# Kernel tuning notes

Hardware: AMD Instinct MI355X
Metric: run time of the kernel (lower is better)

Reference implementation:

```python
import jax, jax.numpy as jnp
import numpy as np

B, N, C, H = 1, 1024, 384, 12
DK, DV, P, PV = 16, 16, 4, 4  # scalar key/value dims, query/value points
POINT_KEY_DIM = 4

def setup_inputs() -> dict:
    key = jax.random.key(0)
    ks = jax.random.split(key, 12)
    s = 0.02
    x = jax.random.normal(ks[0], (B, N, C), dtype=jnp.float32)
    # random orthonormal frames via QR
    A = jax.random.normal(ks[1], (B, N, 3, 3), dtype=jnp.float32)
    rotations, _ = jnp.linalg.qr(A)
    translations = jax.random.normal(ks[2], (B, N, 3), dtype=jnp.float32) * 10.0
    Wq  = jax.random.normal(ks[3], (C, H * DK), dtype=jnp.float32) * s
    Wk  = jax.random.normal(ks[4], (C, H * DK), dtype=jnp.float32) * s
    Wv  = jax.random.normal(ks[5], (C, H * DV), dtype=jnp.float32) * s
    Wqp = jax.random.normal(ks[6], (C, H * P * 3), dtype=jnp.float32) * s
    Wkp = jax.random.normal(ks[7], (C, H * P * 3), dtype=jnp.float32) * s
    Wvp = jax.random.normal(ks[8], (C, H * PV * 3), dtype=jnp.float32) * s
    Wout = jax.random.normal(ks[9], (H * DV + H * PV, C), dtype=jnp.float32) * s
    bout = jnp.zeros((C,), dtype=jnp.float32)
    return {"x": x, "rotations": rotations, "translations": translations,
            "Wq": Wq, "Wk": Wk, "Wv": Wv, "Wqp": Wqp, "Wkp": Wkp, "Wvp": Wvp,
            "Wout": Wout, "bout": bout}

def reference(x, rotations, translations, Wq, Wk, Wv, Wqp, Wkp, Wvp, Wout, bout):
    b, n, c = x.shape
    h = H
    # scalar q/k/v: (b,n,h,d)
    qs = (x @ Wq).reshape(b, n, h, DK)
    ks_ = (x @ Wk).reshape(b, n, h, DK)
    vs = (x @ Wv).reshape(b, n, h, DV)
    # local points: (b,n,h,p,3)
    qp = (x @ Wqp).reshape(b, n, h, P, 3)
    kp = (x @ Wkp).reshape(b, n, h, P, 3)
    vp = (x @ Wvp).reshape(b, n, h, PV, 3)
    t = translations[:, :, None, None, :]
    # rotate to global frame
    qpg = jnp.einsum('bnij,bnhpj->bnhpi', rotations, qp) + t
    kpg = jnp.einsum('bnij,bnhpj->bnhpi', rotations, kp) + t
    vpg = jnp.einsum('bnij,bnhpj->bnhpi', rotations, vp) + t
    # scalar attention logits (b,h,i,j)
    attn_scalar = jnp.einsum('bihd,bjhd->bhij', qs, ks_)
    # squared distances summed over points and coords, expanded to avoid (n,n,h,p,3) diff tensor
    q2 = (qpg ** 2).sum((-1, -2))          # (b,n,h)
    k2 = (kpg ** 2).sum((-1, -2))          # (b,n,h)
    qk = jnp.einsum('bihpc,bjhpc->bhij', qpg, kpg)
    dist_sq = (q2.transpose(0, 2, 1)[:, :, :, None]
               + k2.transpose(0, 2, 1)[:, :, None, :]
               - 2.0 * qk)                 # (b,h,i,j)
    gamma = np.sqrt(2.0 / (9.0 * POINT_KEY_DIM)).astype(np.float32)
    inv_sqrt_dk = np.float32(1.0 / np.sqrt(DK))
    logits = (attn_scalar - 0.5 * gamma * dist_sq) * inv_sqrt_dk
    w = jax.nn.softmax(logits, axis=-1)    # (b,h,i,j)
    # scalar output: (b,n,h*dv)
    out_scalar = jnp.einsum('bhij,bjhd->bihd', w, vs).reshape(b, n, h * DV)
    # point output in global frame, then back to local frame of residue i
    out_pts_g = jnp.einsum('bhij,bjhpc->bihpc', w, vpg)   # (b,n,h,pv,3)
    centered = out_pts_g - t
    out_pts_local = jnp.einsum('bnji,bnhpj->bnhpi', rotations, centered)
    out_pts_norm = jnp.sqrt((out_pts_local ** 2).sum(-1)).reshape(b, n, h * PV)
    out = jnp.concatenate([out_scalar, out_pts_norm], axis=-1)
    return out @ Wout + bout
```

## Files before the change

kernel.cpp:

```cpp
#include <hip/hip_runtime.h>
#include <math.h>

#define N_TOK 1024
#define C_DIM 384
#define H_NUM 12
#define PCOLS 1024
#define Q0 0
#define K0 192
#define V0 384
#define QP0 576
#define KP0 720
#define VP0 864
#define ATT_W 240
#define COEF 0.11785113019775792f
#define ISD 0.25f
#define CC2 (COEF * ISD)
#define NZ 4
#define OKV_V16 896
#define OKV_VP 1408
#define OKV_K2 2176
#define TILE_U 2240
#define TILE_PAD 2304

typedef _Float16 f16x2 __attribute__((ext_vector_type(2)));
typedef __fp16   p16x2 __attribute__((ext_vector_type(2)));
union U32H2 { unsigned int u; f16x2 f; p16x2 p; };
__device__ __forceinline__ f16x2 as_h2(unsigned int v) { U32H2 x; x.u = v; return x.f; }
__device__ __forceinline__ unsigned int pkh(float a, float b) {
    U32H2 x; x.p = __builtin_amdgcn_cvt_pkrtz(a, b); return x.u;
}
__device__ __forceinline__ f16x2 pkf(float a, float b) {
    U32H2 x; x.p = __builtin_amdgcn_cvt_pkrtz(a, b); return x.f;
}

__global__ __launch_bounds__(512) void k_proj(
    const float* __restrict__ x,
    const float* __restrict__ Wq, const float* __restrict__ Wk, const float* __restrict__ Wv,
    const float* __restrict__ Wqp, const float* __restrict__ Wkp, const float* __restrict__ Wvp,
    float* __restrict__ P)
{
    __shared__ unsigned int xs[8][72];
    __shared__ unsigned int wsh[8][64];
    int tid = threadIdx.x;
    int i0 = blockIdx.x * 64, c0 = blockIdx.y * 64;
    int sdp = tid & 7, slr = tid >> 3;
    int wdp = tid >> 6, wcc = tid & 63;
    int ty = tid >> 4, tx = tid & 15;

    int col = c0 + wcc;
    const float* Wb; int od, cb;
    if (col < 192)       { Wb = Wq;  od = 192; cb = col; }
    else if (col < 384)  { Wb = Wk;  od = 192; cb = col - 192; }
    else if (col < 576)  { Wb = Wv;  od = 192; cb = col - 384; }
    else if (col < 720)  { Wb = Wqp; od = 144; cb = col - 576; }
    else if (col < 864)  { Wb = Wkp; od = 144; cb = col - 720; }
    else if (col < 1008) { Wb = Wvp; od = 144; cb = col - 864; }
    else                 { Wb = nullptr; od = 0; cb = 0; }

    const float* xr = x + (i0 + slr) * C_DIM;

    float2 xa = *(const float2*)(xr + sdp * 2);
    float w0 = Wb ? Wb[(2 * wdp) * od + cb] : 0.f;
    float w1 = Wb ? Wb[(2 * wdp + 1) * od + cb] : 0.f;
    float acc[2][4] = {};

    for (int it = 0; it < 24; ++it) {
        xs[sdp][slr] = pkh(xa.x, xa.y);
        wsh[wdp][wcc] = pkh(w0, w1);
        __syncthreads();
        if (it < 23) {
            xa = *(const float2*)(xr + (it + 1) * 16 + sdp * 2);
            w0 = Wb ? Wb[((it + 1) * 16 + 2 * wdp) * od + cb] : 0.f;
            w1 = Wb ? Wb[((it + 1) * 16 + 2 * wdp + 1) * od + cb] : 0.f;
        }
#pragma unroll
        for (int dp = 0; dp < 8; ++dp) {
            uint2 au = *(const uint2*)&xs[dp][ty * 2];
            uint4 bu = *(const uint4*)&wsh[dp][tx * 4];
            unsigned int aa[2] = {au.x, au.y};
            unsigned int bb[4] = {bu.x, bu.y, bu.z, bu.w};
#pragma unroll
            for (int r = 0; r < 2; ++r)
#pragma unroll
                for (int c = 0; c < 4; ++c)
                    acc[r][c] = __builtin_amdgcn_fdot2(as_h2(aa[r]), as_h2(bb[c]), acc[r][c], false);
        }
        __syncthreads();
    }
#pragma unroll
    for (int r = 0; r < 2; ++r)
        *(float4*)(P + (i0 + ty * 2 + r) * PCOLS + c0 + tx * 4) =
            make_float4(acc[r][0], acc[r][1], acc[r][2], acc[r][3]);
}

__global__ __launch_bounds__(256) void k_prep(
    const float* __restrict__ P, const float* __restrict__ rot, const float* __restrict__ trans,
    unsigned int* __restrict__ KVT, unsigned int* __restrict__ Qh, float* __restrict__ qcg)
{
    __shared__ float kb[29 * 128];
    __shared__ float qb[28 * 128];
    __shared__ float vb[28 * 128];
    __shared__ float qcb[128];
    int h = blockIdx.y, nb = blockIdx.x;
    int tid = threadIdx.x;
    int nl = tid & 127, role = tid >> 7;
    int n = nb * 128 + nl;
    const float* R = rot + n * 9;
    float R00 = R[0], R01 = R[1], R02 = R[2];
    float R10 = R[3], R11 = R[4], R12 = R[5];
    float R20 = R[6], R21 = R[7], R22 = R[8];
    float t0 = trans[n * 3 + 0], t1 = trans[n * 3 + 1], t2 = trans[n * 3 + 2];

    if (role == 0) {
        const float* kr = P + n * PCOLS + K0 + h * 16;
#pragma unroll
        for (int d = 0; d < 16; ++d) kb[d * 128 + nl] = kr[d];
        const float* kp = P + n * PCOLS + KP0 + h * 12;
        float k2 = 0.f;
#pragma unroll
        for (int pt = 0; pt < 4; ++pt) {
            float p0 = kp[pt * 3 + 0], p1 = kp[pt * 3 + 1], p2 = kp[pt * 3 + 2];
            float g0 = R00 * p0 + R01 * p1 + R02 * p2 + t0;
            float g1 = R10 * p0 + R11 * p1 + R12 * p2 + t1;
            float g2 = R20 * p0 + R21 * p1 + R22 * p2 + t2;
            kb[(16 + pt * 3 + 0) * 128 + nl] = g0;
            kb[(16 + pt * 3 + 1) * 128 + nl] = g1;
            kb[(16 + pt * 3 + 2) * 128 + nl] = g2;
            k2 += g0 * g0 + g1 * g1 + g2 * g2;
        }
        kb[28 * 128 + nl] = -CC2 * k2;
    } else {
        const float* qr = P + n * PCOLS + Q0 + h * 16;
#pragma unroll
        for (int d = 0; d < 16; ++d) qb[d * 128 + nl] = qr[d] * ISD;
        const float* qp = P + n * PCOLS + QP0 + h * 12;
        float q2 = 0.f;
#pragma unroll
        for (int pt = 0; pt < 4; ++pt) {
            float p0 = qp[pt * 3 + 0], p1 = qp[pt * 3 + 1], p2 = qp[pt * 3 + 2];
            float g0 = R00 * p0 + R01 * p1 + R02 * p2 + t0;
            float g1 = R10 * p0 + R11 * p1 + R12 * p2 + t1;
            float g2 = R20 * p0 + R21 * p1 + R22 * p2 + t2;
            qb[(16 + pt * 3 + 0) * 128 + nl] = g0 * (2.f * CC2);
            qb[(16 + pt * 3 + 1) * 128 + nl] = g1 * (2.f * CC2);
            qb[(16 + pt * 3 + 2) * 128 + nl] = g2 * (2.f * CC2);
            q2 += g0 * g0 + g1 * g1 + g2 * g2;
        }
        qcb[nl] = fmaf(-CC2, q2, -4.0f);
        const float* vr = P + n * PCOLS + V0 + h * 16;
#pragma unroll
        for (int d = 0; d < 16; ++d) vb[d * 128 + nl] = vr[d];
        const float* vp = P + n * PCOLS + VP0 + h * 12;
#pragma unroll
        for (int pt = 0; pt < 4; ++pt) {
            float p0 = vp[pt * 3 + 0], p1 = vp[pt * 3 + 1], p2 = vp[pt * 3 + 2];
            vb[(16 + pt * 3 + 0) * 128 + nl] = R00 * p0 + R01 * p1 + R02 * p2 + t0;
            vb[(16 + pt * 3 + 1) * 128 + nl] = R10 * p0 + R11 * p1 + R12 * p2 + t1;
            vb[(16 + pt * 3 + 2) * 128 + nl] = R20 * p0 + R21 * p1 + R22 * p2 + t2;
        }
    }
    __syncthreads();

    for (int u = tid; u < 2 * TILE_PAD; u += 256) {
        int tt = u / TILE_PAD, r = u % TILE_PAD;
        unsigned int val;
        if (r < OKV_V16) {
            int dp = r >> 6, j = r & 63;
            val = pkh(kb[(2 * dp) * 128 + tt * 64 + j], kb[(2 * dp + 1) * 128 + tt * 64 + j]);
        } else if (r < OKV_VP) {
            int idx = r - OKV_V16;
            int d = idx >> 5, jp = idx & 31;
            val = pkh(vb[d * 128 + tt * 64 + 2 * jp], vb[d * 128 + tt * 64 + 2 * jp + 1]);
        } else if (r < OKV_K2) {
            int idx = r - OKV_VP;
            int d = idx >> 6, j = idx & 63;
            val = __float_as_uint(vb[(16 + d) * 128 + tt * 64 + j]);
        } else if (r < TILE_U) {
            int j = r - OKV_K2;
            val = __float_as_uint(kb[28 * 128 + tt * 64 + j]);
        } else {
            val = 0u;
        }
        KVT[(h * 16 + nb * 2 + tt) * TILE_PAD + r] = val;
    }
    for (int u = tid; u < 14 * 128; u += 256) {
        int dp = u >> 7, n2 = u & 127;
        Qh[(h * 14 + dp) * 1024 + nb * 128 + n2] =
            pkh(qb[(2 * dp) * 128 + n2], qb[(2 * dp + 1) * 128 + n2]);
    }
    if (tid < 32) *(float4*)&qcg[h * 1024 + nb * 128 + tid * 4] = *(float4*)&qcb[tid * 4];
}

__global__ __launch_bounds__(256, 2) void k_attn(
    const unsigned int* __restrict__ KVT, const unsigned int* __restrict__ Qh,
    const float* __restrict__ qcg, float* __restrict__ part)
{
    __shared__ unsigned int KV[2][TILE_PAD];
    __shared__ float red[29 * 64];
    int tid = threadIdx.x;
    int lane = tid & 63, w = tid >> 6;
    int ty = tid >> 3, tx = tid & 7;

    int bid = blockIdx.x;
    int xcd = bid & 7, slot = bid >> 3;
    int pair = xcd * 6 + (slot >> 4);
    int bx = slot & 15;
    int h = pair % H_NUM;
    int z = pair / H_NUM;

    int i0 = bx * 64;
    const unsigned int* KVbase = KVT + (h * 16 + z * 4) * TILE_PAD;

    f16x2 q0p[14], q1p[14];
#pragma unroll
    for (int dp = 0; dp < 14; ++dp) {
        q0p[dp] = as_h2(Qh[(h * 14 + dp) * 1024 + i0 + ty * 2 + 0]);
        q1p[dp] = as_h2(Qh[(h * 14 + dp) * 1024 + i0 + ty * 2 + 1]);
    }
    float qc[2];
    {
        float2 qcv = *(const float2*)&qcg[h * 1024 + i0 + ty * 2];
        qc[0] = qcv.x; qc[1] = qcv.y;
    }

    int nst = (w == 0) ? 3 : 2;
    int gbase = (w == 0) ? 0 : 1 + w * 2;
#define STAGE(T) do { unsigned int* buf_ = KV[(T) & 1];                          \
        const unsigned int* sb_ = KVbase + (T) * TILE_PAD;                       \
        for (int m_ = 0; m_ < nst; ++m_) {                                       \
            int g_ = gbase + m_;                                                 \
            const unsigned int* src_ = sb_ + g_ * 256 + lane * 4;                \
            unsigned int* dst_ = buf_ + g_ * 256;                                \
            __builtin_amdgcn_global_load_lds(                                    \
                (const __attribute__((address_space(1))) void*)src_,             \
                (__attribute__((address_space(3))) void*)dst_, 16, 0, 0);        \
        } } while (0)

    STAGE(0);
    __syncthreads();

    float out[2][28] = {};
    float denom[2] = {};

    for (int t = 0; t < 4; ++t) {
        if (t < 3) STAGE(t + 1);
        const unsigned int* Kb = KV[t & 1];

        float s[2][8] = {};
#pragma unroll
        for (int dp = 0; dp < 14; ++dp) {
            uint4 a = *(const uint4*)&Kb[dp * 64 + tx * 8];
            uint4 b = *(const uint4*)&Kb[dp * 64 + tx * 8 + 4];
            unsigned int ka[8] = {a.x, a.y, a.z, a.w, b.x, b.y, b.z, b.w};
#pragma unroll
            for (int j = 0; j < 8; ++j) {
                s[0][j] = __builtin_amdgcn_fdot2(q0p[dp], as_h2(ka[j]), s[0][j], false);
                s[1][j] = __builtin_amdgcn_fdot2(q1p[dp], as_h2(ka[j]), s[1][j], false);
            }
        }
        const float* k2p = (const float*)&Kb[OKV_K2];
        float4 c0 = *(const float4*)&k2p[tx * 8];
        float4 c1 = *(const float4*)&k2p[tx * 8 + 4];
        float k2v[8] = {c0.x, c0.y, c0.z, c0.w, c1.x, c1.y, c1.z, c1.w};

        float p[2][8];
#pragma unroll
        for (int r = 0; r < 2; ++r) {
#pragma unroll
            for (int j = 0; j < 8; ++j) {
                p[r][j] = __expf(s[r][j] + k2v[j] + qc[r]);
                denom[r] += p[r][j];
            }
        }
        f16x2 pp[2][4];
#pragma unroll
        for (int r = 0; r < 2; ++r)
#pragma unroll
            for (int jp = 0; jp < 4; ++jp)
                pp[r][jp] = pkf(p[r][2 * jp], p[r][2 * jp + 1]);

#pragma unroll
        for (int d = 0; d < 16; ++d) {
            uint4 vv = *(const uint4*)&Kb[OKV_V16 + d * 32 + tx * 4];
#pragma unroll
            for (int r = 0; r < 2; ++r) {
                float acc = out[r][d];
                acc = __builtin_amdgcn_fdot2(pp[r][0], as_h2(vv.x), acc, false);
                acc = __builtin_amdgcn_fdot2(pp[r][1], as_h2(vv.y), acc, false);
                acc = __builtin_amdgcn_fdot2(pp[r][2], as_h2(vv.z), acc, false);
                acc = __builtin_amdgcn_fdot2(pp[r][3], as_h2(vv.w), acc, false);
                out[r][d] = acc;
            }
        }
#pragma unroll
        for (int d = 0; d < 12; ++d) {
            const float* vp = (const float*)&Kb[OKV_VP + d * 64];
            float4 v0 = *(const float4*)&vp[tx * 8];
            float4 v1 = *(const float4*)&vp[tx * 8 + 4];
            float va[8] = {v0.x, v0.y, v0.z, v0.w, v1.x, v1.y, v1.z, v1.w};
#pragma unroll
            for (int r = 0; r < 2; ++r) {
                float acc = out[r][16 + d];
#pragma unroll
                for (int j = 0; j < 8; ++j) acc = fmaf(p[r][j], va[j], acc);
                out[r][16 + d] = acc;
            }
        }
        __syncthreads();
    }

#pragma unroll
    for (int m = 1; m <= 4; m <<= 1) {
#pragma unroll
        for (int r = 0; r < 2; ++r) {
#pragma unroll
            for (int d = 0; d < 28; ++d) out[r][d] += __shfl_xor(out[r][d], m, 64);
            denom[r] += __shfl_xor(denom[r], m, 64);
        }
    }
    if (tx == 0) {
#pragma unroll
        for (int r = 0; r < 2; ++r) {
#pragma unroll
            for (int d = 0; d < 28; ++d) red[d * 64 + ty * 2 + r] = out[r][d];
            red[28 * 64 + ty * 2 + r] = denom[r];
        }
    }
    __syncthreads();
    for (int u = tid; u < 29 * 64; u += 256) {
        part[((z * H_NUM + h) * 29 + (u >> 6)) * N_TOK + i0 + (u & 63)] = red[u];
    }
}

__global__ __launch_bounds__(256) void k_comb(
    const float* __restrict__ part, const float* __restrict__ rot,
    const float* __restrict__ trans, float* __restrict__ att)
{
    int t = blockIdx.x * 256 + threadIdx.x;
    int h = t >> 10, i = t & 1023;
    float v[29];
#pragma unroll
    for (int c = 0; c < 29; ++c) {
        float s = 0.f;
#pragma unroll
        for (int z = 0; z < NZ; ++z)
            s += part[((z * H_NUM + h) * 29 + c) * N_TOK + i];
        v[c] = s;
    }
    float inv = 1.f / v[28];
    float* arow = att + i * ATT_W;
#pragma unroll
    for (int d = 0; d < 16; ++d) arow[h * 16 + d] = v[d] * inv;
    float t0 = trans[i * 3 + 0], t1 = trans[i * 3 + 1], t2v = trans[i * 3 + 2];
    const float* R = rot + i * 9;
#pragma unroll
    for (int p = 0; p < 4; ++p) {
        float c0 = v[16 + p * 3 + 0] * inv - t0;
        float c1 = v[16 + p * 3 + 1] * inv - t1;
        float c2 = v[16 + p * 3 + 2] * inv - t2v;
        float l0 = R[0] * c0 + R[3] * c1 + R[6] * c2;
        float l1 = R[1] * c0 + R[4] * c1 + R[7] * c2;
        float l2 = R[2] * c0 + R[5] * c1 + R[8] * c2;
        arow[192 + h * 4 + p] = sqrtf(l0 * l0 + l1 * l1 + l2 * l2);
    }
}

__global__ __launch_bounds__(256) void k_out(
    const float* __restrict__ att, const float* __restrict__ Wout,
    const float* __restrict__ bout, float* __restrict__ out)
{
    __shared__ float xs[64][17];
    __shared__ float wsh[16][64];
    int tid = threadIdx.x;
    int i0 = blockIdx.x * 64, c0 = blockIdx.y * 64;
    int lr = tid >> 2, lk = (tid & 3) * 4;
    int wr = tid >> 4, wc = (tid & 15) * 4;
    int ty = tid >> 4, tx = tid & 15;

    float4 xa = *(const float4*)(att + (i0 + lr) * ATT_W + lk);
    float4 wa = *(const float4*)(Wout + wr * C_DIM + c0 + wc);
    float acc[4][4] = {};

    for (int it = 0; it < 15; ++it) {
        xs[lr][lk + 0] = xa.x; xs[lr][lk + 1] = xa.y;
        xs[lr][lk + 2] = xa.z; xs[lr][lk + 3] = xa.w;
        *(float4*)&wsh[wr][wc] = wa;
        __syncthreads();
        if (it < 14) {
            xa = *(const float4*)(att + (i0 + lr) * ATT_W + (it + 1) * 16 + lk);
            wa = *(const float4*)(Wout + ((it + 1) * 16 + wr) * C_DIM + c0 + wc);
        }
#pragma unroll
        for (int kk = 0; kk < 16; ++kk) {
            float4 b = *(float4*)&wsh[kk][tx * 4];
            float a0 = xs[ty * 4 + 0][kk];
            float a1 = xs[ty * 4 + 1][kk];
            float a2 = xs[ty * 4 + 2][kk];
            float a3 = xs[ty * 4 + 3][kk];
            acc[0][0] = fmaf(a0, b.x, acc[0][0]); acc[0][1] = fmaf(a0, b.y, acc[0][1]);
            acc[0][2] = fmaf(a0, b.z, acc[0][2]); acc[0][3] = fmaf(a0, b.w, acc[0][3]);
            acc[1][0] = fmaf(a1, b.x, acc[1][0]); acc[1][1] = fmaf(a1, b.y, acc[1][1]);
            acc[1][2] = fmaf(a1, b.z, acc[1][2]); acc[1][3] = fmaf(a1, b.w, acc[1][3]);
            acc[2][0] = fmaf(a2, b.x, acc[2][0]); acc[2][1] = fmaf(a2, b.y, acc[2][1]);
            acc[2][2] = fmaf(a2, b.z, acc[2][2]); acc[2][3] = fmaf(a2, b.w, acc[2][3]);
            acc[3][0] = fmaf(a3, b.x, acc[3][0]); acc[3][1] = fmaf(a3, b.y, acc[3][1]);
            acc[3][2] = fmaf(a3, b.z, acc[3][2]); acc[3][3] = fmaf(a3, b.w, acc[3][3]);
        }
        __syncthreads();
    }
    float4 bb = *(const float4*)(bout + c0 + tx * 4);
#pragma unroll
    for (int r = 0; r < 4; ++r) {
        *(float4*)(out + (i0 + ty * 4 + r) * C_DIM + c0 + tx * 4) =
            make_float4(acc[r][0] + bb.x, acc[r][1] + bb.y, acc[r][2] + bb.z, acc[r][3] + bb.w);
    }
}

extern "C" void kernel_launch(void* const* d_in, const int* in_sizes, int n_in,
                              void* d_out, int out_size, void* d_ws, size_t ws_size,
                              hipStream_t stream) {
    const float* x     = (const float*)d_in[0];
    const float* rot   = (const float*)d_in[1];
    const float* trans = (const float*)d_in[2];
    const float* Wq    = (const float*)d_in[3];
    const float* Wk    = (const float*)d_in[4];
    const float* Wv    = (const float*)d_in[5];
    const float* Wqp   = (const float*)d_in[6];
    const float* Wkp   = (const float*)d_in[7];
    const float* Wvp   = (const float*)d_in[8];
    const float* Wout  = (const float*)d_in[9];
    const float* bout  = (const float*)d_in[10];
    float* out = (float*)d_out;

    float* ws = (float*)d_ws;
    float* P            = ws;
    unsigned int* KVT   = (unsigned int*)(P + N_TOK * PCOLS);
    unsigned int* Qh    = KVT + H_NUM * 16 * TILE_PAD;
    float* qcg          = (float*)(Qh + H_NUM * 14 * 1024);
    float* part         = qcg + H_NUM * 1024;
    float* att          = part + NZ * H_NUM * 29 * 1024;

    k_proj<<<dim3(16, 16), 512, 0, stream>>>(x, Wq, Wk, Wv, Wqp, Wkp, Wvp, P);
    k_prep<<<dim3(8, 12), 256, 0, stream>>>(P, rot, trans, KVT, Qh, qcg);
    k_attn<<<768, 256, 0, stream>>>(KVT, Qh, qcg, part);
    k_comb<<<48, 256, 0, stream>>>(part, rot, trans, att);
    k_out<<<dim3(16, 6), 256, 0, stream>>>(att, Wout, bout, out);
}
```

Before: 81.15 us.

## Fuse partial-combine into output projection and split prep across more blocks

```diff
diff --git a/kernel.cpp b/kernel.cpp
--- a/kernel.cpp
+++ b/kernel.cpp
@@ -97,14 +97,14 @@
     const float* __restrict__ P, const float* __restrict__ rot, const float* __restrict__ trans,
     unsigned int* __restrict__ KVT, unsigned int* __restrict__ Qh, float* __restrict__ qcg)
 {
-    __shared__ float kb[29 * 128];
-    __shared__ float qb[28 * 128];
-    __shared__ float vb[28 * 128];
-    __shared__ float qcb[128];
+    __shared__ float kb[29 * 64];
+    __shared__ float qb[28 * 64];
+    __shared__ float vb[28 * 64];
+    __shared__ float qcb[64];
     int h = blockIdx.y, nb = blockIdx.x;
     int tid = threadIdx.x;
-    int nl = tid & 127, role = tid >> 7;
-    int n = nb * 128 + nl;
+    int nl = tid & 63, role = tid >> 6;
+    int n = nb * 64 + nl;
     const float* R = rot + n * 9;
     float R00 = R[0], R01 = R[1], R02 = R[2];
     float R10 = R[3], R11 = R[4], R12 = R[5];
@@ -114,7 +114,7 @@
     if (role == 0) {
         const float* kr = P + n * PCOLS + K0 + h * 16;
 #pragma unroll
-        for (int d = 0; d < 16; ++d) kb[d * 128 + nl] = kr[d];
+        for (int d = 0; d < 16; ++d) kb[d * 64 + nl] = kr[d];
         const float* kp = P + n * PCOLS + KP0 + h * 12;
         float k2 = 0.f;
 #pragma unroll
@@ -123,16 +123,16 @@
             float g0 = R00 * p0 + R01 * p1 + R02 * p2 + t0;
             float g1 = R10 * p0 + R11 * p1 + R12 * p2 + t1;
             float g2 = R20 * p0 + R21 * p1 + R22 * p2 + t2;
-            kb[(16 + pt * 3 + 0) * 128 + nl] = g0;
-            kb[(16 + pt * 3 + 1) * 128 + nl] = g1;
-            kb[(16 + pt * 3 + 2) * 128 + nl] = g2;
+            kb[(16 + pt * 3 + 0) * 64 + nl] = g0;
+            kb[(16 + pt * 3 + 1) * 64 + nl] = g1;
+            kb[(16 + pt * 3 + 2) * 64 + nl] = g2;
             k2 += g0 * g0 + g1 * g1 + g2 * g2;
         }
-        kb[28 * 128 + nl] = -CC2 * k2;
-    } else {
+        kb[28 * 64 + nl] = -CC2 * k2;
+    } else if (role == 1) {
         const float* qr = P + n * PCOLS + Q0 + h * 16;
 #pragma unroll
-        for (int d = 0; d < 16; ++d) qb[d * 128 + nl] = qr[d] * ISD;
+        for (int d = 0; d < 16; ++d) qb[d * 64 + nl] = qr[d] * ISD;
         const float* qp = P + n * PCOLS + QP0 + h * 12;
         float q2 = 0.f;
 #pragma unroll
@@ -141,54 +141,56 @@
             float g0 = R00 * p0 + R01 * p1 + R02 * p2 + t0;
             float g1 = R10 * p0 + R11 * p1 + R12 * p2 + t1;
             float g2 = R20 * p0 + R21 * p1 + R22 * p2 + t2;
-            qb[(16 + pt * 3 + 0) * 128 + nl] = g0 * (2.f * CC2);
-            qb[(16 + pt * 3 + 1) * 128 + nl] = g1 * (2.f * CC2);
-            qb[(16 + pt * 3 + 2) * 128 + nl] = g2 * (2.f * CC2);
+            qb[(16 + pt * 3 + 0) * 64 + nl] = g0 * (2.f * CC2);
+            qb[(16 + pt * 3 + 1) * 64 + nl] = g1 * (2.f * CC2);
+            qb[(16 + pt * 3 + 2) * 64 + nl] = g2 * (2.f * CC2);
             q2 += g0 * g0 + g1 * g1 + g2 * g2;
         }
         qcb[nl] = fmaf(-CC2, q2, -4.0f);
+    } else if (role == 2) {
         const float* vr = P + n * PCOLS + V0 + h * 16;
 #pragma unroll
-        for (int d = 0; d < 16; ++d) vb[d * 128 + nl] = vr[d];
+        for (int d = 0; d < 16; ++d) vb[d * 64 + nl] = vr[d];
+    } else {
         const float* vp = P + n * PCOLS + VP0 + h * 12;
 #pragma unroll
         for (int pt = 0; pt < 4; ++pt) {
             float p0 = vp[pt * 3 + 0], p1 = vp[pt * 3 + 1], p2 = vp[pt * 3 + 2];
-            vb[(16 + pt * 3 + 0) * 128 + nl] = R00 * p0 + R01 * p1 + R02 * p2 + t0;
-            vb[(16 + pt * 3 + 1) * 128 + nl] = R10 * p0 + R11 * p1 + R12 * p2 + t1;
-            vb[(16 + pt * 3 + 2) * 128 + nl] = R20 * p0 + R21 * p1 + R22 * p2 + t2;
+            vb[(16 + pt * 3 + 0) * 64 + nl] = R00 * p0 + R01 * p1 + R02 * p2 + t0;
+            vb[(16 + pt * 3 + 1) * 64 + nl] = R10 * p0 + R11 * p1 + R12 * p2 + t1;
+            vb[(16 + pt * 3 + 2) * 64 + nl] = R20 * p0 + R21 * p1 + R22 * p2 + t2;
         }
     }
     __syncthreads();
 
-    for (int u = tid; u < 2 * TILE_PAD; u += 256) {
-        int tt = u / TILE_PAD, r = u % TILE_PAD;
+    unsigned int* dstT = KVT + (h * 16 + nb) * TILE_PAD;
+    for (int r = tid; r < TILE_PAD; r += 256) {
         unsigned int val;
         if (r < OKV_V16) {
             int dp = r >> 6, j = r & 63;
-            val = pkh(kb[(2 * dp) * 128 + tt * 64 + j], kb[(2 * dp + 1) * 128 + tt * 64 + j]);
+            val = pkh(kb[(2 * dp) * 64 + j], kb[(2 * dp + 1) * 64 + j]);
         } else if (r < OKV_VP) {
             int idx = r - OKV_V16;
             int d = idx >> 5, jp = idx & 31;
-            val = pkh(vb[d * 128 + tt * 64 + 2 * jp], vb[d * 128 + tt * 64 + 2 * jp + 1]);
+            val = pkh(vb[d * 64 + 2 * jp], vb[d * 64 + 2 * jp + 1]);
         } else if (r < OKV_K2) {
             int idx = r - OKV_VP;
             int d = idx >> 6, j = idx & 63;
-            val = __float_as_uint(vb[(16 + d) * 128 + tt * 64 + j]);
+            val = __float_as_uint(vb[(16 + d) * 64 + j]);
         } else if (r < TILE_U) {
             int j = r - OKV_K2;
-            val = __float_as_uint(kb[28 * 128 + tt * 64 + j]);
+            val = __float_as_uint(kb[28 * 64 + j]);
         } else {
             val = 0u;
         }
-        KVT[(h * 16 + nb * 2 + tt) * TILE_PAD + r] = val;
-    }
-    for (int u = tid; u < 14 * 128; u += 256) {
-        int dp = u >> 7, n2 = u & 127;
-        Qh[(h * 14 + dp) * 1024 + nb * 128 + n2] =
-            pkh(qb[(2 * dp) * 128 + n2], qb[(2 * dp + 1) * 128 + n2]);
-    }
-    if (tid < 32) *(float4*)&qcg[h * 1024 + nb * 128 + tid * 4] = *(float4*)&qcb[tid * 4];
+        dstT[r] = val;
+    }
+    for (int u = tid; u < 14 * 64; u += 256) {
+        int dp = u >> 6, n2 = u & 63;
+        Qh[(h * 14 + dp) * 1024 + nb * 64 + n2] =
+            pkh(qb[(2 * dp) * 64 + n2], qb[(2 * dp + 1) * 64 + n2]);
+    }
+    if (tid < 16) *(float4*)&qcg[h * 1024 + nb * 64 + tid * 4] = *(float4*)&qcb[tid * 4];
 }
 
 __global__ __launch_bounds__(256, 2) void k_attn(
@@ -332,71 +334,77 @@
     }
 }
 
-__global__ __launch_bounds__(256) void k_comb(
+__global__ __launch_bounds__(256) void k_outc(
     const float* __restrict__ part, const float* __restrict__ rot,
-    const float* __restrict__ trans, float* __restrict__ att)
-{
-    int t = blockIdx.x * 256 + threadIdx.x;
-    int h = t >> 10, i = t & 1023;
-    float v[29];
-#pragma unroll
-    for (int c = 0; c < 29; ++c) {
-        float s = 0.f;
-#pragma unroll
-        for (int z = 0; z < NZ; ++z)
-            s += part[((z * H_NUM + h) * 29 + c) * N_TOK + i];
-        v[c] = s;
-    }
-    float inv = 1.f / v[28];
-    float* arow = att + i * ATT_W;
-#pragma unroll
-    for (int d = 0; d < 16; ++d) arow[h * 16 + d] = v[d] * inv;
-    float t0 = trans[i * 3 + 0], t1 = trans[i * 3 + 1], t2v = trans[i * 3 + 2];
-    const float* R = rot + i * 9;
-#pragma unroll
-    for (int p = 0; p < 4; ++p) {
-        float c0 = v[16 + p * 3 + 0] * inv - t0;
-        float c1 = v[16 + p * 3 + 1] * inv - t1;
-        float c2 = v[16 + p * 3 + 2] * inv - t2v;
-        float l0 = R[0] * c0 + R[3] * c1 + R[6] * c2;
-        float l1 = R[1] * c0 + R[4] * c1 + R[7] * c2;
-        float l2 = R[2] * c0 + R[5] * c1 + R[8] * c2;
-        arow[192 + h * 4 + p] = sqrtf(l0 * l0 + l1 * l1 + l2 * l2);
-    }
-}
-
-__global__ __launch_bounds__(256) void k_out(
-    const float* __restrict__ att, const float* __restrict__ Wout,
+    const float* __restrict__ trans, const float* __restrict__ Wout,
     const float* __restrict__ bout, float* __restrict__ out)
 {
-    __shared__ float xs[64][17];
+    __shared__ float ab[64][241];
+    __shared__ float den[64][13];
     __shared__ float wsh[16][64];
     int tid = threadIdx.x;
     int i0 = blockIdx.x * 64, c0 = blockIdx.y * 64;
-    int lr = tid >> 2, lk = (tid & 3) * 4;
+
+    for (int u = tid; u < 64 * 12; u += 256) {
+        int r = u & 63, h = u >> 6;
+        float s = 0.f;
+#pragma unroll
+        for (int z = 0; z < NZ; ++z)
+            s += part[((z * H_NUM + h) * 29 + 28) * N_TOK + i0 + r];
+        den[r][h] = 1.f / s;
+    }
+    __syncthreads();
+
+    for (int u = tid; u < 192 * 64; u += 256) {
+        int c = u >> 6, r = u & 63;
+        int h = c >> 4, d = c & 15;
+        float s = 0.f;
+#pragma unroll
+        for (int z = 0; z < NZ; ++z)
+            s += part[((z * H_NUM + h) * 29 + d) * N_TOK + i0 + r];
+        ab[r][c] = s * den[r][h];
+    }
+    for (int u = tid; u < 48 * 64; u += 256) {
+        int pc = u >> 6, r = u & 63;
+        int h = pc >> 2, p = pc & 3;
+        int i = i0 + r;
+        float inv = den[r][h];
+        float v0 = 0.f, v1 = 0.f, v2 = 0.f;
+#pragma unroll
+        for (int z = 0; z < NZ; ++z) {
+            int base = ((z * H_NUM + h) * 29 + 16 + p * 3) * N_TOK + i;
+            v0 += part[base];
+            v1 += part[base + N_TOK];
+            v2 += part[base + 2 * N_TOK];
+        }
+        float c0f = v0 * inv - trans[i * 3 + 0];
+        float c1f = v1 * inv - trans[i * 3 + 1];
+        float c2f = v2 * inv - trans[i * 3 + 2];
+        const float* R = rot + i * 9;
+        float l0 = R[0] * c0f + R[3] * c1f + R[6] * c2f;
+        float l1 = R[1] * c0f + R[4] * c1f + R[7] * c2f;
+        float l2 = R[2] * c0f + R[5] * c1f + R[8] * c2f;
+        ab[r][192 + pc] = sqrtf(l0 * l0 + l1 * l1 + l2 * l2);
+    }
+
     int wr = tid >> 4, wc = (tid & 15) * 4;
     int ty = tid >> 4, tx = tid & 15;
-
-    float4 xa = *(const float4*)(att + (i0 + lr) * ATT_W + lk);
     float4 wa = *(const float4*)(Wout + wr * C_DIM + c0 + wc);
     float acc[4][4] = {};
+    __syncthreads();
 
     for (int it = 0; it < 15; ++it) {
-        xs[lr][lk + 0] = xa.x; xs[lr][lk + 1] = xa.y;
-        xs[lr][lk + 2] = xa.z; xs[lr][lk + 3] = xa.w;
         *(float4*)&wsh[wr][wc] = wa;
         __syncthreads();
-        if (it < 14) {
-            xa = *(const float4*)(att + (i0 + lr) * ATT_W + (it + 1) * 16 + lk);
+        if (it < 14)
             wa = *(const float4*)(Wout + ((it + 1) * 16 + wr) * C_DIM + c0 + wc);
-        }
 #pragma unroll
         for (int kk = 0; kk < 16; ++kk) {
             float4 b = *(float4*)&wsh[kk][tx * 4];
-            float a0 = xs[ty * 4 + 0][kk];
-            float a1 = xs[ty * 4 + 1][kk];
-            float a2 = xs[ty * 4 + 2][kk];
-            float a3 = xs[ty * 4 + 3][kk];
+            float a0 = ab[ty * 4 + 0][it * 16 + kk];
+            float a1 = ab[ty * 4 + 1][it * 16 + kk];
+            float a2 = ab[ty * 4 + 2][it * 16 + kk];
+            float a3 = ab[ty * 4 + 3][it * 16 + kk];
             acc[0][0] = fmaf(a0, b.x, acc[0][0]); acc[0][1] = fmaf(a0, b.y, acc[0][1]);
             acc[0][2] = fmaf(a0, b.z, acc[0][2]); acc[0][3] = fmaf(a0, b.w, acc[0][3]);
             acc[1][0] = fmaf(a1, b.x, acc[1][0]); acc[1][1] = fmaf(a1, b.y, acc[1][1]);
@@ -438,11 +446,9 @@
     unsigned int* Qh    = KVT + H_NUM * 16 * TILE_PAD;
     float* qcg          = (float*)(Qh + H_NUM * 14 * 1024);
     float* part         = qcg + H_NUM * 1024;
-    float* att          = part + NZ * H_NUM * 29 * 1024;
 
     k_proj<<<dim3(16, 16), 512, 0, stream>>>(x, Wq, Wk, Wv, Wqp, Wkp, Wvp, P);
-    k_prep<<<dim3(8, 12), 256, 0, stream>>>(P, rot, trans, KVT, Qh, qcg);
+    k_prep<<<dim3(16, 12), 256, 0, stream>>>(P, rot, trans, KVT, Qh, qcg);
     k_attn<<<768, 256, 0, stream>>>(KVT, Qh, qcg, part);
-    k_comb<<<48, 256, 0, stream>>>(part, rot, trans, att);
-    k_out<<<dim3(16, 6), 256, 0, stream>>>(att, Wout, bout, out);
-}
+    k_outc<<<dim3(16, 6), 256, 0, stream>>>(part, rot, trans, Wout, bout, out);
+}
```

Result: no change. 79.97 us (median of 2 runs) (-1.5%).
